# Kernel optimization log

Hardware: AMD Instinct MI355X
Metric: run time of the kernel (lower is better)

## Reference

```python
import jax, jax.numpy as jnp
import numpy as np

# Module constants (match init_kwargs)
IMG_W = 384
IMG_H = 384
DECAY = 0.97
VEH_W = 2.1
VEH_L = 4.9
PPM = 5
LIGHT_OFF_X = 12.0
LIGHT_OFF_Y = 3.25
ALPHA = 1.1


def create_coordinate_mask(nx, ny, ppm):
    # Metric coordinates of every BEV pixel, ego frame origin at image center.
    xs = (jnp.arange(nx, dtype=jnp.float32) - nx / 2.0) / ppm
    ys = (jnp.arange(ny, dtype=jnp.float32) - ny / 2.0) / ppm
    X, Y = jnp.meshgrid(xs, ys)  # (ny, nx)
    return jnp.stack([X, Y], axis=-1)  # (H, W, 2)


def rotate_batched(location, yaw):
    # Express future poses (t=1..T-1) in the frame of the pose at t=0.
    loc0 = location[:, :1]              # (B,1,2)
    yaw0 = yaw[:, :1]                   # (B,1,1)
    rel = location[:, 1:] - loc0        # (B,T-1,2)
    c, s = jnp.cos(yaw0), jnp.sin(yaw0)
    x = c * rel[..., 0:1] + s * rel[..., 1:2]    # (B,T-1,1)
    y = -s * rel[..., 0:1] + c * rel[..., 1:2]   # (B,T-1,1)
    return x, y, yaw[:, 1:] - yaw0


def align_with_ego(x, y, yaw, cm):
    # Translate grid to ego position then rotate into ego heading frame.
    # x,y,yaw: (B,T-1,1); cm: (H,W,2). Returns two (B,T-1,H,W) coord fields.
    relx = cm[..., 0][None, None] - x[..., None]   # (B,T-1,H,W)
    rely = cm[..., 1][None, None] - y[..., None]
    c = jnp.cos(yaw)[..., None]
    s = jnp.sin(yaw)[..., None]
    ax = c * relx + s * rely
    ay = -s * relx + c * rely
    return ax, ay


def calculate_mask(ax, ay, dx, dy, vw, vl, alpha):
    dtype = ax.dtype
    # Speed-dependent corridor ahead of the vehicle.
    mask_car = ((jnp.abs(ax) <= dx) & (ay >= 0.0) & (ay <= dy)).astype(dtype)
    # Inflated vehicle footprint (for lane / offroad costs).
    mask_side = ((jnp.abs(ax) <= alpha * vw / 2.0)
                 & (jnp.abs(ay) <= alpha * vl / 2.0)).astype(dtype)
    return mask_car, mask_side


def setup_inputs() -> dict:
    key = jax.random.key(0)
    k1, k2, k3, k4 = jax.random.split(key, 4)
    B, T = 8, 11
    location = jax.random.normal(k1, (B, T, 2), dtype=jnp.float32) * 5.0
    yaw = jax.random.normal(k2, (B, T, 1), dtype=jnp.float32) * 0.3
    speed = jax.random.uniform(k3, (B, T, 1), dtype=jnp.float32) * 15.0
    bev = jax.random.uniform(k4, (B, T, 8, IMG_H, IMG_W), dtype=jnp.float32)
    return {"location": location, "yaw": yaw, "speed": speed, "bev": bev}


def reference(location, yaw, speed, bev):
    cm = create_coordinate_mask(IMG_W, IMG_H, PPM)   # (H,W,2)
    x, y, yaw_ = rotate_batched(location, yaw)        # (B,T-1,1) each
    speed_ = speed[:, 1:, 0:1]                        # (B,T-1,1)

    ax, ay = align_with_ego(x, y, yaw_, cm)
    axl, ayl = align_with_ego(x + LIGHT_OFF_X, y + LIGHT_OFF_Y, yaw_, cm)

    dx = VEH_W / 2.0 + 4.0
    dx_light = VEH_W + 1.0
    dy = (1.5 * (jnp.maximum(10.0, speed_) + VEH_L) + 1.0)[..., None]  # (B,T-1,1,1)
    dy_light = (speed_ * 0.5 + VEH_L * 3.0)[..., None]                  # (B,T-1,1,1)

    mask_car, mask_side = calculate_mask(ax, ay, dx, dy, VEH_W, VEH_L, ALPHA)
    mask_light, _ = calculate_mask(axl, ayl, dx_light, dy_light, VEH_W, VEH_L, ALPHA)

    # Binarize BEV at 0.5 (matches the in-place > / <= thresholding).
    bev_b = (bev[:, 1:] > 0.5).astype(bev.dtype)  # (B,T-1,8,H,W)

    Tm1 = bev_b.shape[1]
    decay = jnp.power(jnp.float32(DECAY),
                      jnp.arange(Tm1, dtype=jnp.float32)).reshape(1, Tm1, 1, 1)

    def cost(chan, mask):
        return jnp.sum(bev_b[:, :, chan] * mask * decay)

    lane_cost = cost(1, mask_side)
    vehicle_cost = cost(2, mask_car)
    green_light_cost = cost(3, mask_light)
    yellow_light_cost = cost(4, mask_light)
    red_light_cost = cost(5, mask_light)
    pedestrian_cost = cost(6, mask_car)
    offroad_cost = cost(7, mask_side)

    return (lane_cost, vehicle_cost, green_light_cost, yellow_light_cost,
            red_light_cost, pedestrian_cost, offroad_cost,
            mask_car, mask_side, mask_light)
```

## Files before the change

### kernel.cpp

```cpp
#include <hip/hip_runtime.h>
#include <math.h>

constexpr int IMG     = 384;
constexpr int NPIX    = IMG * IMG;
constexpr int TM1     = 10;
constexpr int NIMG    = 80;
constexpr int THREADS = 256;
constexpr int GPT     = 4;
constexpr int GPB     = THREADS * GPT;
constexpr int NGRP    = NPIX / 4;
constexpr int NBX     = NGRP / GPB;
constexpr long long NMASK = (long long)NIMG * NPIX;

typedef float v4f __attribute__((ext_vector_type(4)));


__global__ __launch_bounds__(THREADS) void cost_main(
    const float* __restrict__ loc,
    const float* __restrict__ yaw,
    const float* __restrict__ speed,
    const float* __restrict__ bev,
    float* __restrict__ out)
{
    const int img = blockIdx.y;
    const int b   = img / TM1;
    const int t   = img - b * TM1;
    const int tid = threadIdx.x;

    const float yaw0 = yaw[b * 11];
    const float c0 = cosf(yaw0), s0 = sinf(yaw0);
    const float rx = loc[(b * 11 + t + 1) * 2 + 0] - loc[b * 22 + 0];
    const float ry = loc[(b * 11 + t + 1) * 2 + 1] - loc[b * 22 + 1];
    const float x0 =  c0 * rx + s0 * ry;
    const float y0 = -s0 * rx + c0 * ry;
    const float yw = yaw[b * 11 + t + 1] - yaw0;
    const float c = cosf(yw), s = sinf(yw);
    const float sp  = speed[b * 11 + t + 1];
    const float dy  = 1.5f * (fmaxf(10.0f, sp) + 4.9f) + 1.0f;
    const float dyl = sp * 0.5f + 14.7f;
    const float ox  = 12.0f * c + 3.25f * s;
    const float oy  = 12.0f * s - 3.25f * c;

    const float* bp = bev + (size_t)((b * 11 + t + 1) * 8) * NPIX;
    float* ocar   = out + 7 + (size_t)img * NPIX;
    float* oside  = ocar + NMASK;
    float* olight = ocar + 2 * NMASK;

    float aL = 0.f, aV = 0.f, aG = 0.f, aY = 0.f, aR = 0.f, aP = 0.f, aO = 0.f;

    const int g0 = blockIdx.x * GPB + tid;
    #pragma unroll
    for (int it = 0; it < GPT; ++it) {
        const int g = g0 + it * THREADS;
        if (g != NGRP - 1) {
            const int pb = 4 * g + 1;
            float mc[4], ms[4], ml[4];
            #pragma unroll
            for (int k = 0; k < 4; ++k) {
                const int p = pb + k;
                const int i = p / IMG;
                const int j = p - i * IMG;
                const float X = (float)j * 0.2f - 38.4f;
                const float Y = (float)i * 0.2f - 38.4f;
                const float relx = X - x0, rely = Y - y0;
                const float ax = c * relx + s * rely;
                const float ay = c * rely - s * relx;
                const float axl = ax - ox, ayl = ay + oy;
                mc[k] = (fabsf(ax)  <= 5.05f  && ay >= 0.f && ay <= dy)   ? 1.f : 0.f;
                ms[k] = (fabsf(ax)  <= 1.155f && fabsf(ay) <= 2.695f)     ? 1.f : 0.f;
                ml[k] = (fabsf(axl) <= 3.1f   && ayl >= 0.f && ayl <= dyl)? 1.f : 0.f;
            }
            v4f vc = {mc[0], mc[1], mc[2], mc[3]};
            v4f vs = {ms[0], ms[1], ms[2], ms[3]};
            v4f vl = {ml[0], ml[1], ml[2], ml[3]};
            *(v4f*)(ocar + pb)   = vc;
            *(v4f*)(oside + pb)  = vs;
            *(v4f*)(olight + pb) = vl;

            if (ms[0] + ms[1] + ms[2] + ms[3] > 0.f) {
                #pragma unroll
                for (int k = 0; k < 4; ++k) {
                    aL += ms[k] * ((bp[1 * NPIX + pb + k] > 0.5f) ? 1.f : 0.f);
                    aO += ms[k] * ((bp[7 * NPIX + pb + k] > 0.5f) ? 1.f : 0.f);
                }
            }
            if (mc[0] + mc[1] + mc[2] + mc[3] > 0.f) {
                #pragma unroll
                for (int k = 0; k < 4; ++k) {
                    aV += mc[k] * ((bp[2 * NPIX + pb + k] > 0.5f) ? 1.f : 0.f);
                    aP += mc[k] * ((bp[6 * NPIX + pb + k] > 0.5f) ? 1.f : 0.f);
                }
            }
            if (ml[0] + ml[1] + ml[2] + ml[3] > 0.f) {
                #pragma unroll
                for (int k = 0; k < 4; ++k) {
                    aG += ml[k] * ((bp[3 * NPIX + pb + k] > 0.5f) ? 1.f : 0.f);
                    aY += ml[k] * ((bp[4 * NPIX + pb + k] > 0.5f) ? 1.f : 0.f);
                    aR += ml[k] * ((bp[5 * NPIX + pb + k] > 0.5f) ? 1.f : 0.f);
                }
            }
        } else {
            const int pp[4] = {0, NPIX - 3, NPIX - 2, NPIX - 1};
            for (int k = 0; k < 4; ++k) {
                const int p = pp[k];
                const int i = p / IMG;
                const int j = p - i * IMG;
                const float X = (float)j * 0.2f - 38.4f;
                const float Y = (float)i * 0.2f - 38.4f;
                const float relx = X - x0, rely = Y - y0;
                const float ax = c * relx + s * rely;
                const float ay = c * rely - s * relx;
                const float axl = ax - ox, ayl = ay + oy;
                const float mc = (fabsf(ax)  <= 5.05f  && ay >= 0.f && ay <= dy)    ? 1.f : 0.f;
                const float msd= (fabsf(ax)  <= 1.155f && fabsf(ay) <= 2.695f)      ? 1.f : 0.f;
                const float ml = (fabsf(axl) <= 3.1f   && ayl >= 0.f && ayl <= dyl) ? 1.f : 0.f;
                ocar[p] = mc; oside[p] = msd; olight[p] = ml;
                if (msd > 0.f) {
                    aL += (bp[1 * NPIX + p] > 0.5f) ? 1.f : 0.f;
                    aO += (bp[7 * NPIX + p] > 0.5f) ? 1.f : 0.f;
                }
                if (mc > 0.f) {
                    aV += (bp[2 * NPIX + p] > 0.5f) ? 1.f : 0.f;
                    aP += (bp[6 * NPIX + p] > 0.5f) ? 1.f : 0.f;
                }
                if (ml > 0.f) {
                    aG += (bp[3 * NPIX + p] > 0.5f) ? 1.f : 0.f;
                    aY += (bp[4 * NPIX + p] > 0.5f) ? 1.f : 0.f;
                    aR += (bp[5 * NPIX + p] > 0.5f) ? 1.f : 0.f;
                }
            }
        }
    }

    float acc[7] = {aL, aV, aG, aY, aR, aP, aO};
    #pragma unroll
    for (int k = 0; k < 7; ++k) {
        #pragma unroll
        for (int off = 32; off > 0; off >>= 1)
            acc[k] += __shfl_down(acc[k], off, 64);
    }

    __shared__ float red[4][7];
    const int wid = tid >> 6, lane = tid & 63;
    if (lane == 0) {
        #pragma unroll
        for (int k = 0; k < 7; ++k) red[wid][k] = acc[k];
    }
    __syncthreads();
    if (tid < 7) {
        const float v = red[0][tid] + red[1][tid] + red[2][tid] + red[3][tid];
        if (v != 0.0f) {
            float decay = 1.0f;
            for (int q = 0; q < t; ++q) decay *= 0.97f;
            atomicAdd(&out[tid], v * decay);
        }
    }
}

extern "C" void kernel_launch(void* const* d_in, const int* in_sizes, int n_in,
                              void* d_out, int out_size, void* d_ws, size_t ws_size,
                              hipStream_t stream) {
    const float* loc   = (const float*)d_in[0];
    const float* yaw   = (const float*)d_in[1];
    const float* speed = (const float*)d_in[2];
    const float* bev   = (const float*)d_in[3];
    float* out = (float*)d_out;

    (void)hipMemsetAsync(d_out, 0, 7 * sizeof(float), stream);

    dim3 grid(NBX, NIMG);
    cost_main<<<grid, THREADS, 0, stream>>>(loc, yaw, speed, bev, out);
}
```

Measured before the change: 39.57 us.

## Split mask writing from cost sums using per-row analytic mask intervals

Per image, the kernel now computes in double precision, for each row and mask plane, a conservative column interval where the rotated rectangle can be nonzero. Writer blocks store zeros only outside those intervals. Twelve extra blocks per image walk only the columns inside the intervals, computing exact masks, writing them and summing the BEV channels. This avoids computing masks and reading BEV for pixels far from the vehicle footprints. The cost is double-precision setup, per-row serial loops in the summing blocks, and tricky edge handling for the offset pixel groups.

```diff
diff --git a/kernel.cpp b/kernel.cpp
--- a/kernel.cpp
+++ b/kernel.cpp
@@ -10,9 +10,43 @@
 constexpr int GPB     = THREADS * GPT;
 constexpr int NGRP    = NPIX / 4;
 constexpr int NBX     = NGRP / GPB;
+constexpr int NSUM    = 12;
 constexpr long long NMASK = (long long)NIMG * NPIX;
 
 typedef float v4f __attribute__((ext_vector_type(4)));
+
+__device__ __forceinline__ unsigned row_pack(int plane, int r,
+    double c, double s, double x0, double y0,
+    double dy, double dyl, double ox, double oy)
+{
+    double u0, u1, v0, v1;
+    if (plane == 0)      { u0 = -5.05;    u1 = 5.05;     v0 = 0.0;    v1 = dy; }
+    else if (plane == 1) { u0 = -1.155;   u1 = 1.155;    v0 = -2.695; v1 = 2.695; }
+    else                 { u0 = ox - 3.1; u1 = ox + 3.1; v0 = -oy;    v1 = dyl - oy; }
+    const double Yd = (double)r * 0.2 - 38.4;
+    const double mA = c * 0.2;
+    const double qA = c * (-38.4 - x0) + s * (Yd - y0);
+    const double mB = -s * 0.2;
+    const double qB = c * (Yd - y0) + s * (38.4 + x0);
+    double lo = -1e9, hi = 1e9;
+    bool empty = false;
+    if (fabs(mA) > 1e-12) {
+        const double pad = 1e-3 / fabs(mA);
+        const double t0 = (u0 - qA) / mA, t1 = (u1 - qA) / mA;
+        lo = fmax(lo, fmin(t0, t1) - pad);
+        hi = fmin(hi, fmax(t0, t1) + pad);
+    } else if (qA < u0 - 1e-3 || qA > u1 + 1e-3) empty = true;
+    if (fabs(mB) > 1e-12) {
+        const double pad = 1e-3 / fabs(mB);
+        const double t0 = (v0 - qB) / mB, t1 = (v1 - qB) / mB;
+        lo = fmax(lo, fmin(t0, t1) - pad);
+        hi = fmin(hi, fmax(t0, t1) + pad);
+    } else if (qB < v0 - 1e-3 || qB > v1 + 1e-3) empty = true;
+    lo -= 1.0; hi += 1.0;
+    if (empty || hi < 0.0 || lo > 383.0 || lo > hi) return 1000u;
+    lo = fmax(lo, 0.0); hi = fmin(hi, 383.0);
+    return (unsigned)(int)floor(lo) | (((unsigned)(int)ceil(hi)) << 10);
+}
 
 
 __global__ __launch_bounds__(THREADS) void cost_main(
@@ -41,23 +75,93 @@
     const float ox  = 12.0f * c + 3.25f * s;
     const float oy  = 12.0f * s - 3.25f * c;
 
+    const double cd = c, sd = s, x0d = x0, y0d = y0;
+    const double dyd = dy, dyld = dyl, oxd = ox, oyd = oy;
+
+    if (blockIdx.x < NBX) {
+        __shared__ unsigned spk[42];
+        const int g0s = blockIdx.x * GPB;
+        const int rlo = (4 * g0s + 1) / IMG;
+        const int rhi = min(IMG - 1, (4 * (g0s + GPB - 1) + 4) / IMG);
+        const int nent = (rhi - rlo + 2) * 3;
+        for (int idx = tid; idx < nent; idx += THREADS) {
+            const int rr = rlo + idx / 3;
+            const int pl = idx - (idx / 3) * 3;
+            spk[idx] = (rr < IMG) ? row_pack(pl, rr, cd, sd, x0d, y0d,
+                                             dyd, dyld, oxd, oyd)
+                                  : 1000u;
+        }
+        __syncthreads();
+
+        float* base = out + 7 + (size_t)img * NPIX;
+        const v4f z4 = {0.f, 0.f, 0.f, 0.f};
+        const int g0 = g0s + tid;
+        #pragma unroll
+        for (int it = 0; it < GPT; ++it) {
+            const int g = g0 + it * THREADS;
+            if (g == NGRP - 1) continue;
+            const int p1   = 4 * g + 1;
+            const int r    = p1 / IMG;
+            const int col1 = p1 - r * IMG;
+            const int k    = col1 >> 2;
+            const int c4   = col1 + 3;
+            const int ro   = (r - rlo) * 3;
+            #pragma unroll
+            for (int pl = 0; pl < 3; ++pl) {
+                const unsigned pk = spk[ro + pl];
+                const int plo = pk & 1023, phi = (pk >> 10) & 1023;
+                bool skip = (c4 >= plo) && (col1 <= phi);
+                if (k == 95 && r < IMG - 1)
+                    skip = skip || ((spk[ro + 3 + pl] & 1023u) == 0u);
+                if (!skip)
+                    *(v4f*)(base + (size_t)pl * NMASK + p1) = z4;
+            }
+        }
+        return;
+    }
+
+    const int q     = blockIdx.x - NBX;
+    const int plane = q >> 2;
+    const int z     = q & 3;
+
+    __shared__ unsigned spk2[192];
+    for (int idx = tid; idx < 192; idx += THREADS) {
+        const int m  = idx >> 1;
+        const int rr = z + 4 * m + (idx & 1);
+        spk2[idx] = (rr < IMG) ? row_pack(plane, rr, cd, sd, x0d, y0d,
+                                          dyd, dyld, oxd, oyd)
+                               : 1000u;
+    }
+    __syncthreads();
+
     const float* bp = bev + (size_t)((b * 11 + t + 1) * 8) * NPIX;
-    float* ocar   = out + 7 + (size_t)img * NPIX;
-    float* oside  = ocar + NMASK;
-    float* olight = ocar + 2 * NMASK;
-
-    float aL = 0.f, aV = 0.f, aG = 0.f, aY = 0.f, aR = 0.f, aP = 0.f, aO = 0.f;
-
-    const int g0 = blockIdx.x * GPB + tid;
-    #pragma unroll
-    for (int it = 0; it < GPT; ++it) {
-        const int g = g0 + it * THREADS;
-        if (g != NGRP - 1) {
+    float* op = out + 7 + (size_t)img * NPIX + (size_t)plane * NMASK;
+    int chA, chB, chC;
+    if (plane == 0)      { chA = 2; chB = 6; chC = -1; }
+    else if (plane == 1) { chA = 1; chB = 7; chC = -1; }
+    else                 { chA = 3; chB = 4; chC = 5;  }
+
+    float a0 = 0.f, a1 = 0.f, a2 = 0.f;
+
+    for (int m = 0; m < 96; ++m) {
+        const int r = z + 4 * m;
+        const unsigned pk = spk2[2 * m];
+        const int plo = pk & 1023, phi = (pk >> 10) & 1023;
+        int klo = (plo - 1) >> 2; if (klo < 0) klo = 0;
+        int khi = (phi - 1) >> 2; if (khi > 95) khi = 95;
+        int nq  = khi - klo + 1;  if (nq < 0) nq = 0;
+        const bool bit = (r < IMG - 1) && ((spk2[2 * m + 1] & 1023u) == 0u);
+        const bool extra = bit && !(nq > 0 && klo <= 95 && 95 <= khi);
+        const int tot = nq + (extra ? 1 : 0);
+        for (int e = tid; e < tot; e += THREADS) {
+            const int kk = (e < nq) ? (klo + e) : 95;
+            const int g  = 96 * r + kk;
+            if (g == NGRP - 1) continue;
             const int pb = 4 * g + 1;
-            float mc[4], ms[4], ml[4];
+            float mm[4];
             #pragma unroll
-            for (int k = 0; k < 4; ++k) {
-                const int p = pb + k;
+            for (int k2 = 0; k2 < 4; ++k2) {
+                const int p = pb + k2;
                 const int i = p / IMG;
                 const int j = p - i * IMG;
                 const float X = (float)j * 0.2f - 38.4f;
@@ -65,94 +169,80 @@
                 const float relx = X - x0, rely = Y - y0;
                 const float ax = c * relx + s * rely;
                 const float ay = c * rely - s * relx;
-                const float axl = ax - ox, ayl = ay + oy;
-                mc[k] = (fabsf(ax)  <= 5.05f  && ay >= 0.f && ay <= dy)   ? 1.f : 0.f;
-                ms[k] = (fabsf(ax)  <= 1.155f && fabsf(ay) <= 2.695f)     ? 1.f : 0.f;
-                ml[k] = (fabsf(axl) <= 3.1f   && ayl >= 0.f && ayl <= dyl)? 1.f : 0.f;
-            }
-            v4f vc = {mc[0], mc[1], mc[2], mc[3]};
-            v4f vs = {ms[0], ms[1], ms[2], ms[3]};
-            v4f vl = {ml[0], ml[1], ml[2], ml[3]};
-            *(v4f*)(ocar + pb)   = vc;
-            *(v4f*)(oside + pb)  = vs;
-            *(v4f*)(olight + pb) = vl;
-
-            if (ms[0] + ms[1] + ms[2] + ms[3] > 0.f) {
-                #pragma unroll
-                for (int k = 0; k < 4; ++k) {
-                    aL += ms[k] * ((bp[1 * NPIX + pb + k] > 0.5f) ? 1.f : 0.f);
-                    aO += ms[k] * ((bp[7 * NPIX + pb + k] > 0.5f) ? 1.f : 0.f);
+                float mv;
+                if (plane == 0)
+                    mv = (fabsf(ax) <= 5.05f && ay >= 0.f && ay <= dy) ? 1.f : 0.f;
+                else if (plane == 1)
+                    mv = (fabsf(ax) <= 1.155f && fabsf(ay) <= 2.695f) ? 1.f : 0.f;
+                else {
+                    const float axl = ax - ox, ayl = ay + oy;
+                    mv = (fabsf(axl) <= 3.1f && ayl >= 0.f && ayl <= dyl) ? 1.f : 0.f;
+                }
+                mm[k2] = mv;
+                if (mv > 0.f) {
+                    a0 += (bp[chA * NPIX + p] > 0.5f) ? 1.f : 0.f;
+                    a1 += (bp[chB * NPIX + p] > 0.5f) ? 1.f : 0.f;
+                    if (chC >= 0) a2 += (bp[chC * NPIX + p] > 0.5f) ? 1.f : 0.f;
                 }
             }
-            if (mc[0] + mc[1] + mc[2] + mc[3] > 0.f) {
-                #pragma unroll
-                for (int k = 0; k < 4; ++k) {
-                    aV += mc[k] * ((bp[2 * NPIX + pb + k] > 0.5f) ? 1.f : 0.f);
-                    aP += mc[k] * ((bp[6 * NPIX + pb + k] > 0.5f) ? 1.f : 0.f);
-                }
-            }
-            if (ml[0] + ml[1] + ml[2] + ml[3] > 0.f) {
-                #pragma unroll
-                for (int k = 0; k < 4; ++k) {
-                    aG += ml[k] * ((bp[3 * NPIX + pb + k] > 0.5f) ? 1.f : 0.f);
-                    aY += ml[k] * ((bp[4 * NPIX + pb + k] > 0.5f) ? 1.f : 0.f);
-                    aR += ml[k] * ((bp[5 * NPIX + pb + k] > 0.5f) ? 1.f : 0.f);
-                }
-            }
-        } else {
-            const int pp[4] = {0, NPIX - 3, NPIX - 2, NPIX - 1};
-            for (int k = 0; k < 4; ++k) {
-                const int p = pp[k];
-                const int i = p / IMG;
-                const int j = p - i * IMG;
-                const float X = (float)j * 0.2f - 38.4f;
-                const float Y = (float)i * 0.2f - 38.4f;
-                const float relx = X - x0, rely = Y - y0;
-                const float ax = c * relx + s * rely;
-                const float ay = c * rely - s * relx;
-                const float axl = ax - ox, ayl = ay + oy;
-                const float mc = (fabsf(ax)  <= 5.05f  && ay >= 0.f && ay <= dy)    ? 1.f : 0.f;
-                const float msd= (fabsf(ax)  <= 1.155f && fabsf(ay) <= 2.695f)      ? 1.f : 0.f;
-                const float ml = (fabsf(axl) <= 3.1f   && ayl >= 0.f && ayl <= dyl) ? 1.f : 0.f;
-                ocar[p] = mc; oside[p] = msd; olight[p] = ml;
-                if (msd > 0.f) {
-                    aL += (bp[1 * NPIX + p] > 0.5f) ? 1.f : 0.f;
-                    aO += (bp[7 * NPIX + p] > 0.5f) ? 1.f : 0.f;
-                }
-                if (mc > 0.f) {
-                    aV += (bp[2 * NPIX + p] > 0.5f) ? 1.f : 0.f;
-                    aP += (bp[6 * NPIX + p] > 0.5f) ? 1.f : 0.f;
-                }
-                if (ml > 0.f) {
-                    aG += (bp[3 * NPIX + p] > 0.5f) ? 1.f : 0.f;
-                    aY += (bp[4 * NPIX + p] > 0.5f) ? 1.f : 0.f;
-                    aR += (bp[5 * NPIX + p] > 0.5f) ? 1.f : 0.f;
-                }
-            }
-        }
-    }
-
-    float acc[7] = {aL, aV, aG, aY, aR, aP, aO};
+            v4f v = {mm[0], mm[1], mm[2], mm[3]};
+            *(v4f*)(op + pb) = v;
+        }
+    }
+
+    float acc[3] = {a0, a1, a2};
     #pragma unroll
-    for (int k = 0; k < 7; ++k) {
+    for (int k = 0; k < 3; ++k) {
         #pragma unroll
         for (int off = 32; off > 0; off >>= 1)
             acc[k] += __shfl_down(acc[k], off, 64);
     }
-
-    __shared__ float red[4][7];
+    __shared__ float red[4][3];
     const int wid = tid >> 6, lane = tid & 63;
     if (lane == 0) {
         #pragma unroll
-        for (int k = 0; k < 7; ++k) red[wid][k] = acc[k];
+        for (int k = 0; k < 3; ++k) red[wid][k] = acc[k];
     }
     __syncthreads();
-    if (tid < 7) {
+    if (tid < 3) {
         const float v = red[0][tid] + red[1][tid] + red[2][tid] + red[3][tid];
-        if (v != 0.0f) {
-            float decay = 1.0f;
-            for (int q = 0; q < t; ++q) decay *= 0.97f;
-            atomicAdd(&out[tid], v * decay);
+        int slot = -1;
+        if (plane == 0)      slot = (tid == 0) ? 1 : (tid == 1) ? 5 : -1;
+        else if (plane == 1) slot = (tid == 0) ? 0 : (tid == 1) ? 6 : -1;
+        else                 slot = 2 + tid;
+        if (slot >= 0 && v != 0.f) {
+            float decay = 1.f;
+            for (int qd = 0; qd < t; ++qd) decay *= 0.97f;
+            atomicAdd(&out[slot], v * decay);
+        }
+    }
+
+    if (plane == 0 && z == 0 && tid == 0) {
+        float decay = 1.f;
+        for (int qd = 0; qd < t; ++qd) decay *= 0.97f;
+        const int pp[4] = {0, NPIX - 3, NPIX - 2, NPIX - 1};
+        for (int e = 0; e < 4; ++e) {
+            const int p = pp[e];
+            const int i = p / IMG, j = p - i * IMG;
+            const float X = (float)j * 0.2f - 38.4f;
+            const float Y = (float)i * 0.2f - 38.4f;
+            const float relx = X - x0, rely = Y - y0;
+            const float ax = c * relx + s * rely;
+            const float ay = c * rely - s * relx;
+            const float axl = ax - ox, ayl = ay + oy;
+            const float mc  = (fabsf(ax) <= 5.05f  && ay >= 0.f && ay <= dy)   ? 1.f : 0.f;
+            const float msd = (fabsf(ax) <= 1.155f && fabsf(ay) <= 2.695f)     ? 1.f : 0.f;
+            const float mlt = (fabsf(axl) <= 3.1f  && ayl >= 0.f && ayl <= dyl)? 1.f : 0.f;
+            out[7 + (size_t)img * NPIX + p]             = mc;
+            out[7 + (size_t)img * NPIX + NMASK + p]     = msd;
+            out[7 + (size_t)img * NPIX + 2 * NMASK + p] = mlt;
+            if (msd > 0.f) { if (bp[1 * NPIX + p] > 0.5f) atomicAdd(&out[0], decay);
+                             if (bp[7 * NPIX + p] > 0.5f) atomicAdd(&out[6], decay); }
+            if (mc  > 0.f) { if (bp[2 * NPIX + p] > 0.5f) atomicAdd(&out[1], decay);
+                             if (bp[6 * NPIX + p] > 0.5f) atomicAdd(&out[5], decay); }
+            if (mlt > 0.f) { if (bp[3 * NPIX + p] > 0.5f) atomicAdd(&out[2], decay);
+                             if (bp[4 * NPIX + p] > 0.5f) atomicAdd(&out[3], decay);
+                             if (bp[5 * NPIX + p] > 0.5f) atomicAdd(&out[4], decay); }
         }
     }
 }
@@ -168,6 +258,6 @@
 
     (void)hipMemsetAsync(d_out, 0, 7 * sizeof(float), stream);
 
-    dim3 grid(NBX, NIMG);
+    dim3 grid(NBX + NSUM, NIMG);
     cost_main<<<grid, THREADS, 0, stream>>>(loc, yaw, speed, bev, out);
 }
```

Measured after the change: 107.1 us. 2.71x slower.
